# Kernel optimization log

Measured on AMD Instinct MI355X. Metric: run time of the kernel, lower is better.

## Reference

```python
import jax, jax.numpy as jnp
import numpy as np

EPS_COS = 1e-8   # nxn_cos_sim eps
SMOOTH = 1e-4    # DiceLoss smooth
EPS_DICE = 1e-7  # smp soft_dice_score clamp_min eps

BS, C, H, W = 8, 512, 128, 128
K = 512  # codebook / num classes


def setup_inputs() -> dict:
    key = jax.random.key(0)
    k1, k2, k3 = jax.random.split(key, 3)
    output = jax.random.normal(k1, (BS, C, H, W), dtype=jnp.float32)
    embeddings = jax.random.normal(k2, (K, C), dtype=jnp.float32)
    # ground-truth one-hot annotation (bs, K, h, w)
    gt_labels = jax.random.randint(k3, (BS, H, W), 0, K)
    ann_one_hot = jax.nn.one_hot(gt_labels, K, dtype=jnp.float32).transpose(0, 3, 1, 2)
    return {"output": output, "ann_one_hot": ann_one_hot, "embeddings": embeddings}


def reference(output, ann_one_hot, embeddings):
    bs, c, h, w = output.shape
    k = embeddings.shape[0]
    x = output.transpose(0, 2, 3, 1).reshape(-1, c)           # [N, C]
    # nxn cosine similarity [N, K]
    numerator = x @ embeddings.T
    a_l2 = jnp.sum(x * x, axis=1)                              # [N]
    b_l2 = jnp.sum(embeddings * embeddings, axis=1)            # [K]
    denominator = jnp.maximum(jnp.sqrt(a_l2[:, None] * b_l2[None, :]), EPS_COS)
    labels = jnp.argmax(numerator / denominator, axis=-1).reshape(bs, h, w)
    # ann_to_one_hot -> (bs, K, h, w)
    pred_one_hot = jax.nn.one_hot(labels, k, dtype=output.dtype).transpose(0, 3, 1, 2)
    # smp DiceLoss(mode='multilabel', smooth=1e-4, from_logits=False)
    yp = pred_one_hot.reshape(bs, k, -1)
    yt = ann_one_hot.reshape(bs, k, -1).astype(yp.dtype)
    dims = (0, 2)
    intersection = jnp.sum(yp * yt, axis=dims)                 # [K]
    cardinality = jnp.sum(yp + yt, axis=dims)                  # [K]
    score = (2.0 * intersection + SMOOTH) / jnp.maximum(cardinality + SMOOTH, EPS_DICE)
    loss = 1.0 - score
    present = (jnp.sum(yt, axis=dims) > 0).astype(loss.dtype)  # only classes present in GT
    return jnp.mean(loss * present)
```

## Files before the change

### kernel.cpp

```cpp
#include <hip/hip_runtime.h>
#include <hip/hip_bf16.h>

#define BSZ 8
#define CDIM 512
#define KDIM 512
#define HWSZ 16384
#define NPIX (BSZ*HWSZ)

using bf16x8 = __attribute__((ext_vector_type(8))) short;
using f32x4  = __attribute__((ext_vector_type(4))) float;
typedef unsigned long long u64;

__device__ __forceinline__ unsigned pack2bf16(float lo, float hi) {
  return (__builtin_bit_cast(unsigned, lo) >> 16) |
         (__builtin_bit_cast(unsigned, hi) & 0xFFFF0000u);
}

__device__ __forceinline__ void gload_lds16(const unsigned short* g, unsigned short* l) {
  __builtin_amdgcn_global_load_lds(
      (const __attribute__((address_space(1))) unsigned int*)g,
      (__attribute__((address_space(3))) unsigned int*)l, 16, 0, 0);
}

__global__ __launch_bounds__(64) void prep_emb_kernel(const float* __restrict__ E,
                                                      unsigned short* __restrict__ Eb) {
  int k = blockIdx.x;
  int lane = threadIdx.x;
  const float4* row = (const float4*)(E + (size_t)k * CDIM);
  float4 v0 = row[lane * 2], v1 = row[lane * 2 + 1];
  float ss = v0.x*v0.x + v0.y*v0.y + v0.z*v0.z + v0.w*v0.w
           + v1.x*v1.x + v1.y*v1.y + v1.z*v1.z + v1.w*v1.w;
  #pragma unroll
  for (int d = 1; d < 64; d <<= 1) ss += __shfl_xor(ss, d, 64);
  float rinv = rsqrtf(fmaxf(ss, 1e-24f));
  float f[8] = {v0.x, v0.y, v0.z, v0.w, v1.x, v1.y, v1.z, v1.w};
  unsigned o[8];
  #pragma unroll
  for (int e = 0; e < 8; ++e) {
    float x = f[e] * rinv;
    unsigned u = __builtin_bit_cast(unsigned, x);
    o[e] = (u + 0x7FFFu + ((u >> 16) & 1u)) >> 16;
  }
  uint4 pack;
  pack.x = o[0] | (o[1] << 16);
  pack.y = o[2] | (o[3] << 16);
  pack.z = o[4] | (o[5] << 16);
  pack.w = o[6] | (o[7] << 16);
  ((uint4*)(Eb + (size_t)k * CDIM))[lane] = pack;
}

__global__ __launch_bounds__(256) void transpose_gt_kernel(
    const float* __restrict__ X, const float* __restrict__ ANN,
    unsigned short* __restrict__ Xt, float* __restrict__ gt_count) {
  __shared__ unsigned int lds[64 * 65];
  __shared__ float sw[4];
  int t = threadIdx.x;
  int bid = blockIdx.x;
  int pb = bid & 2047, cb = bid >> 11;
  int px0 = pb * 64, c0 = cb * 128;
  int b = px0 >> 14, hw = px0 & (HWSZ - 1);
  int p = t & 15, cg = t >> 4;

  const float* xs = X + ((size_t)b * CDIM + c0) * HWSZ + hw + 4 * p;
  float4 v[8];
  #pragma unroll
  for (int j = 0; j < 4; ++j) {
    const float* s = xs + (size_t)(2 * (cg + 16 * j)) * HWSZ;
    v[2 * j]     = *(const float4*)s;
    v[2 * j + 1] = *(const float4*)(s + HWSZ);
  }
  const float* Ap = ANN + (size_t)bid * 8192 + t * 4;
  float s0 = 0.f;
  #pragma unroll
  for (int r = 0; r < 8; ++r) {
    float4 a4 = *(const float4*)(Ap + r * 1024);
    s0 += (a4.x + a4.y) + (a4.z + a4.w);
  }
  #pragma unroll
  for (int j = 0; j < 4; ++j) {
    float f0[4] = {v[2*j].x, v[2*j].y, v[2*j].z, v[2*j].w};
    float f1[4] = {v[2*j+1].x, v[2*j+1].y, v[2*j+1].z, v[2*j+1].w};
    #pragma unroll
    for (int jj = 0; jj < 4; ++jj)
      lds[(4 * p + jj) * 65 + cg + 16 * j] = pack2bf16(f0[jj], f1[jj]);
  }
  __syncthreads();
  #pragma unroll
  for (int k2 = 0; k2 < 4; ++k2) {
    int ch = t + 256 * k2;
    int px = ch >> 4, j = ch & 15;
    uint4 o;
    o.x = lds[px * 65 + 4 * j];
    o.y = lds[px * 65 + 4 * j + 1];
    o.z = lds[px * 65 + 4 * j + 2];
    o.w = lds[px * 65 + 4 * j + 3];
    *(uint4*)(Xt + (size_t)(px0 + px) * CDIM + c0 + 8 * j) = o;
  }
  #pragma unroll
  for (int d = 1; d < 64; d <<= 1) s0 += __shfl_xor(s0, d, 64);
  if ((t & 63) == 0) sw[t >> 6] = s0;
  __syncthreads();
  if (t == 0) atomicAdd(&gt_count[(bid >> 1) & (KDIM - 1)], sw[0] + sw[1] + sw[2] + sw[3]);
}

__global__ __launch_bounds__(256, 4) void gemm_argmax_kernel(
    const unsigned short* __restrict__ Xt, const unsigned short* __restrict__ Eb,
    u64* __restrict__ keys) {
  __shared__ unsigned short As[2][128 * 32];
  __shared__ unsigned short Bs[2][128 * 32];
  int t = threadIdx.x;
  int lane = t & 63;
  int wv = t >> 6;
  int p15 = lane & 15, q = lane >> 4;
  int wr = wv >> 1, wc = wv & 1;
  int bid = (blockIdx.x & 7) * 512 + (blockIdx.x >> 3);
  int px0  = (bid >> 2) * 128;
  int cls0 = (bid & 3) * 128;

  int ubase = (t & ~63) * 8;
  #define STAGE(buf, i)                                                              \
    {                                                                                \
      _Pragma("unroll")                                                              \
      for (int j = 0; j < 2; ++j) {                                                  \
        int ch = t + 256 * j;                                                        \
        int row = ch >> 2, q4 = ch & 3;                                              \
        gload_lds16(Xt + (size_t)(px0 + row) * CDIM + (i) * 32 + q4 * 8,             \
                    &As[buf][ubase + j * 2048]);                                     \
        gload_lds16(Eb + (size_t)(cls0 + row) * CDIM + (i) * 32 + q4 * 8,            \
                    &Bs[buf][ubase + j * 2048]);                                     \
      }                                                                              \
    }

  f32x4 acc[4][4];
  #pragma unroll
  for (int m = 0; m < 4; ++m)
    #pragma unroll
    for (int n = 0; n < 4; ++n)
      acc[m][n] = (f32x4){0.f, 0.f, 0.f, 0.f};

  STAGE(0, 0);
  for (int i = 0; i < 16; ++i) {
    int cur = i & 1;
    if (i < 15) STAGE(cur ^ 1, i + 1);
    __syncthreads();
    bf16x8 a[4], bfr[4];
    #pragma unroll
    for (int m = 0; m < 4; ++m)
      a[m] = *(bf16x8*)&As[cur][(wr * 64 + m * 16 + p15) * 32 + q * 8];
    #pragma unroll
    for (int n = 0; n < 4; ++n)
      bfr[n] = *(bf16x8*)&Bs[cur][(wc * 64 + n * 16 + p15) * 32 + q * 8];
    #pragma unroll
    for (int n = 0; n < 4; ++n)
      #pragma unroll
      for (int m = 0; m < 4; ++m)
        acc[m][n] = __builtin_amdgcn_mfma_f32_16x16x32_bf16(a[m], bfr[n], acc[m][n], 0, 0, 0);
    __syncthreads();
  }
  #undef STAGE

  #pragma unroll
  for (int m = 0; m < 4; ++m) {
    #pragma unroll
    for (int r = 0; r < 4; ++r) {
      float best = acc[m][0][r];
      int bn = 0;
      #pragma unroll
      for (int n = 1; n < 4; ++n) {
        float v = acc[m][n][r];
        if (v > best) { best = v; bn = n; }
      }
      int bk = cls0 + wc * 64 + bn * 16 + p15;
      #pragma unroll
      for (int d = 1; d < 16; d <<= 1) {
        float ov = __shfl_xor(best, d, 64);
        int   ok = __shfl_xor(bk, d, 64);
        if (ov > best || (ov == best && ok < bk)) { best = ov; bk = ok; }
      }
      if (p15 == 0) {
        int px = px0 + wr * 64 + m * 16 + q * 4 + r;
        unsigned u = __builtin_bit_cast(unsigned, best);
        unsigned ou = u ^ ((unsigned)((int)u >> 31) | 0x80000000u);
        u64 key = ((u64)ou << 32) | (unsigned)(511 - bk);
        atomicMax(&keys[px], key);
      }
    }
  }
}

__global__ __launch_bounds__(256) void count_kernel(
    const u64* __restrict__ keys, const float* __restrict__ ANN,
    int* __restrict__ pred_count, int* __restrict__ inter) {
  int px = blockIdx.x * 256 + threadIdx.x;
  u64 key = keys[px];
  int cls = 511 - (int)(unsigned)(key & 0xFFFFFFFFull);
  atomicAdd(&pred_count[cls], 1);
  int b = px >> 14, hw = px & (HWSZ - 1);
  float g = ANN[((size_t)b * KDIM + cls) * HWSZ + hw];
  if (g > 0.5f) atomicAdd(&inter[cls], 1);
}

__global__ __launch_bounds__(512) void final_kernel(
    const int* __restrict__ pred_count, const int* __restrict__ inter,
    const float* __restrict__ gt_count, float* __restrict__ out) {
  int k = threadIdx.x;
  float G = gt_count[k];
  float P = (float)pred_count[k];
  float I = (float)inter[k];
  float card  = P + G;
  float score = (2.f * I + 1e-4f) / fmaxf(card + 1e-4f, 1e-7f);
  float v = (G > 0.f) ? (1.f - score) : 0.f;
  #pragma unroll
  for (int d = 1; d < 64; d <<= 1) v += __shfl_xor(v, d, 64);
  __shared__ float sw[8];
  if ((k & 63) == 0) sw[k >> 6] = v;
  __syncthreads();
  if (k == 0) {
    float s = 0.f;
    #pragma unroll
    for (int i = 0; i < 8; ++i) s += sw[i];
    out[0] = s / (float)KDIM;
  }
}

__global__ __launch_bounds__(256) void gt_count_fb(const float* __restrict__ ANN,
                                                   float* __restrict__ gt_count) {
  int slice = blockIdx.x;
  int k = slice & (KDIM - 1);
  const float4* p = (const float4*)(ANN + (size_t)slice * HWSZ);
  float s = 0.f;
  #pragma unroll
  for (int i = 0; i < 16; ++i) {
    float4 v = p[threadIdx.x + i * 256];
    s += v.x + v.y + v.z + v.w;
  }
  #pragma unroll
  for (int d = 1; d < 64; d <<= 1) s += __shfl_xor(s, d, 64);
  __shared__ float sw[4];
  if ((threadIdx.x & 63) == 0) sw[threadIdx.x >> 6] = s;
  __syncthreads();
  if (threadIdx.x == 0) atomicAdd(&gt_count[k], sw[0] + sw[1] + sw[2] + sw[3]);
}

__global__ __launch_bounds__(256, 1) void gemm_fb(
    const float* __restrict__ X, const float* __restrict__ ANN,
    const unsigned short* __restrict__ Eb,
    int* __restrict__ pred_count, int* __restrict__ inter) {
  int tid = threadIdx.x;
  int wv = tid >> 6;
  int lane = tid & 63;
  int p15 = lane & 15, q = lane >> 4;
  int pix0 = blockIdx.x * 64;
  int b = pix0 >> 14;
  int hw = pix0 & (HWSZ - 1);
  const float*          Xb = X  + (size_t)b * CDIM * HWSZ + hw + p15;
  const unsigned short* Ew = Eb + (size_t)(wv * 128) * CDIM;
  f32x4 acc[4][8];
  #pragma unroll
  for (int m = 0; m < 4; ++m)
    #pragma unroll
    for (int n = 0; n < 8; ++n)
      acc[m][n] = (f32x4){0.f, 0.f, 0.f, 0.f};
  for (int cs = 0; cs < 16; ++cs) {
    int c0 = cs * 32 + q * 8;
    bf16x8 a[4];
    #pragma unroll
    for (int m = 0; m < 4; ++m)
      #pragma unroll
      for (int e = 0; e < 8; ++e) {
        float x = Xb[(size_t)(c0 + e) * HWSZ + m * 16];
        a[m][e] = (short)(__builtin_bit_cast(unsigned, x) >> 16);
      }
    bf16x8 bfrag[8];
    #pragma unroll
    for (int n = 0; n < 8; ++n)
      bfrag[n] = *(const bf16x8*)(Ew + (size_t)(n * 16 + p15) * CDIM + cs * 32 + q * 8);
    #pragma unroll
    for (int n = 0; n < 8; ++n)
      #pragma unroll
      for (int m = 0; m < 4; ++m)
        acc[m][n] = __builtin_amdgcn_mfma_f32_16x16x32_bf16(a[m], bfrag[n], acc[m][n], 0, 0, 0);
  }
  __shared__ float s_v[4][64];
  __shared__ int   s_k[4][64];
  #pragma unroll
  for (int m = 0; m < 4; ++m)
    #pragma unroll
    for (int r = 0; r < 4; ++r) {
      float best = acc[m][0][r];
      int bn = 0;
      #pragma unroll
      for (int n = 1; n < 8; ++n) {
        float v = acc[m][n][r];
        if (v > best) { best = v; bn = n; }
      }
      int bk = wv * 128 + bn * 16 + p15;
      #pragma unroll
      for (int d = 1; d < 16; d <<= 1) {
        float ov = __shfl_xor(best, d, 64);
        int   ok = __shfl_xor(bk, d, 64);
        if (ov > best || (ov == best && ok < bk)) { best = ov; bk = ok; }
      }
      if (p15 == 0) {
        int p = m * 16 + q * 4 + r;
        s_v[wv][p] = best;
        s_k[wv][p] = bk;
      }
    }
  __syncthreads();
  if (tid < 64) {
    int p = tid;
    float best = s_v[0][p]; int bk = s_k[0][p];
    #pragma unroll
    for (int w = 1; w < 4; ++w) {
      float v = s_v[w][p]; int kk = s_k[w][p];
      if (v > best || (v == best && kk < bk)) { best = v; bk = kk; }
    }
    atomicAdd(&pred_count[bk], 1);
    float g = ANN[((size_t)b * KDIM + bk) * HWSZ + hw + p];
    if (g > 0.5f) atomicAdd(&inter[bk], 1);
  }
}

extern "C" void kernel_launch(void* const* d_in, const int* in_sizes, int n_in,
                              void* d_out, int out_size, void* d_ws, size_t ws_size,
                              hipStream_t stream) {
  const float* X   = (const float*)d_in[0];
  const float* ANN = (const float*)d_in[1];
  const float* E   = (const float*)d_in[2];

  char* base = (char*)d_ws;
  unsigned short* Eb = (unsigned short*)base;
  float* gt_count    = (float*)(base + 524288);
  int*   pred_count  = (int*)  (base + 524288 + 2048);
  int*   inter       = (int*)  (base + 524288 + 4096);
  u64*   keys        = (u64*)  (base + 1048576);
  unsigned short* Xt = (unsigned short*)(base + 2097152);

  size_t need = 2097152 + (size_t)NPIX * CDIM * 2;

  prep_emb_kernel<<<KDIM, 64, 0, stream>>>(E, Eb);
  if (ws_size >= need) {
    hipMemsetAsync(base + 524288, 0, 1048576 + 524288 - 524288 + 1048576, stream);
    transpose_gt_kernel<<<8192, 256, 0, stream>>>(X, ANN, Xt, gt_count);
    gemm_argmax_kernel<<<4096, 256, 0, stream>>>(Xt, Eb, keys);
    count_kernel<<<NPIX / 256, 256, 0, stream>>>(keys, ANN, pred_count, inter);
  } else {
    hipMemsetAsync(base + 524288, 0, 6144, stream);
    gt_count_fb<<<BSZ * KDIM, 256, 0, stream>>>(ANN, gt_count);
    gemm_fb<<<NPIX / 64, 256, 0, stream>>>(X, ANN, Eb, pred_count, inter);
  }
  final_kernel<<<1, 512, 0, stream>>>(pred_count, inter, gt_count, (float*)d_out);
}
```

Baseline: 292.6 us.

## Pre-tile Xt and embeddings into GEMM-block-contiguous layout for linear staging loads

The transpose kernel now writes bf16 activations in a tiled layout, 128-pixel blocks by 32-channel slices stored contiguously. The embedding prep also writes a matching tiled copy. The GEMM staging loads then become fully contiguous 8KB chunks per k-step instead of strided row reads. The transpose kernel is also restructured to 256-pixel by 64-channel tiles, using half as many blocks and a different LDS layout. This costs extra workspace and a second embedding write, and depends on the new index math being correct.

```diff
diff --git a/kernel.cpp b/kernel.cpp
--- a/kernel.cpp
+++ b/kernel.cpp
@@ -23,7 +23,8 @@
 }
 
 __global__ __launch_bounds__(64) void prep_emb_kernel(const float* __restrict__ E,
-                                                      unsigned short* __restrict__ Eb) {
+                                                      unsigned short* __restrict__ Eb,
+                                                      unsigned short* __restrict__ EbT) {
   int k = blockIdx.x;
   int lane = threadIdx.x;
   const float4* row = (const float4*)(E + (size_t)k * CDIM);
@@ -47,64 +48,69 @@
   pack.z = o[4] | (o[5] << 16);
   pack.w = o[6] | (o[7] << 16);
   ((uint4*)(Eb + (size_t)k * CDIM))[lane] = pack;
+  int clsb = k >> 7, rowi = k & 127, cs = lane >> 2, q4 = lane & 3;
+  *(uint4*)(EbT + (size_t)clsb * 65536 + cs * 4096 + rowi * 32 + q4 * 8) = pack;
 }
 
 __global__ __launch_bounds__(256) void transpose_gt_kernel(
     const float* __restrict__ X, const float* __restrict__ ANN,
-    unsigned short* __restrict__ Xt, float* __restrict__ gt_count) {
-  __shared__ unsigned int lds[64 * 65];
-  __shared__ float sw[4];
+    unsigned short* __restrict__ XtT, float* __restrict__ gt_count) {
+  __shared__ unsigned int lds[256 * 36];
+  __shared__ float swr[4];
   int t = threadIdx.x;
   int bid = blockIdx.x;
-  int pb = bid & 2047, cb = bid >> 11;
-  int px0 = pb * 64, c0 = cb * 128;
+  int pt = bid & 511, cg = bid >> 9;
+  int px0 = pt * 256, c0 = cg * 64;
   int b = px0 >> 14, hw = px0 & (HWSZ - 1);
-  int p = t & 15, cg = t >> 4;
-
-  const float* xs = X + ((size_t)b * CDIM + c0) * HWSZ + hw + 4 * p;
-  float4 v[8];
-  #pragma unroll
-  for (int j = 0; j < 4; ++j) {
-    const float* s = xs + (size_t)(2 * (cg + 16 * j)) * HWSZ;
-    v[2 * j]     = *(const float4*)s;
-    v[2 * j + 1] = *(const float4*)(s + HWSZ);
-  }
-  const float* Ap = ANN + (size_t)bid * 8192 + t * 4;
+  int w = t >> 6, lane = t & 63;
+
+  const float* xb = X + ((size_t)b * CDIM + c0 + 16 * w) * HWSZ + hw + 4 * lane;
+  const float* Ap = ANN + (size_t)bid * HWSZ + 4 * t;
   float s0 = 0.f;
-  #pragma unroll
-  for (int r = 0; r < 8; ++r) {
-    float4 a4 = *(const float4*)(Ap + r * 1024);
-    s0 += (a4.x + a4.y) + (a4.z + a4.w);
-  }
-  #pragma unroll
-  for (int j = 0; j < 4; ++j) {
-    float f0[4] = {v[2*j].x, v[2*j].y, v[2*j].z, v[2*j].w};
-    float f1[4] = {v[2*j+1].x, v[2*j+1].y, v[2*j+1].z, v[2*j+1].w};
-    #pragma unroll
-    for (int jj = 0; jj < 4; ++jj)
-      lds[(4 * p + jj) * 65 + cg + 16 * j] = pack2bf16(f0[jj], f1[jj]);
-  }
-  __syncthreads();
-  #pragma unroll
-  for (int k2 = 0; k2 < 4; ++k2) {
-    int ch = t + 256 * k2;
-    int px = ch >> 4, j = ch & 15;
-    uint4 o;
-    o.x = lds[px * 65 + 4 * j];
-    o.y = lds[px * 65 + 4 * j + 1];
-    o.z = lds[px * 65 + 4 * j + 2];
-    o.w = lds[px * 65 + 4 * j + 3];
-    *(uint4*)(Xt + (size_t)(px0 + px) * CDIM + c0 + 8 * j) = o;
+
+  #pragma unroll
+  for (int ph = 0; ph < 2; ++ph) {
+    float4 xv[8];
+    #pragma unroll
+    for (int r = 0; r < 4; ++r) {
+      int cc = 2 * (4 * ph + r);
+      xv[2*r]   = *(const float4*)(xb + (size_t)cc * HWSZ);
+      xv[2*r+1] = *(const float4*)(xb + (size_t)(cc + 1) * HWSZ);
+    }
+    #pragma unroll
+    for (int r = 0; r < 8; ++r) {
+      float4 a4 = *(const float4*)(Ap + (size_t)(8 * ph + r) * 1024);
+      s0 += (a4.x + a4.y) + (a4.z + a4.w);
+    }
+    #pragma unroll
+    for (int j = 0; j < 4; ++j) {
+      unsigned pk[4];
+      #pragma unroll
+      for (int r = 0; r < 4; ++r)
+        pk[r] = pack2bf16(((const float*)&xv[2*r])[j], ((const float*)&xv[2*r+1])[j]);
+      *(uint4*)&lds[(size_t)(4 * lane + j) * 36 + 8 * w + 4 * ph] = *(const uint4*)pk;
+    }
+  }
+  __syncthreads();
+  #pragma unroll
+  for (int rr = 0; rr < 8; ++rr) {
+    int ch = rr * 256 + t;
+    int q4 = ch & 3, px = (ch >> 2) & 255, s = ch >> 10;
+    uint4 o = *(const uint4*)&lds[(size_t)px * 36 + s * 16 + q4 * 4];
+    int pxg = px0 + px;
+    int pxb = pxg >> 7, prow = pxg & 127;
+    int ics = cg * 2 + s;
+    *(uint4*)(XtT + (size_t)(pxb * 16 + ics) * 4096 + prow * 32 + q4 * 8) = o;
   }
   #pragma unroll
   for (int d = 1; d < 64; d <<= 1) s0 += __shfl_xor(s0, d, 64);
-  if ((t & 63) == 0) sw[t >> 6] = s0;
-  __syncthreads();
-  if (t == 0) atomicAdd(&gt_count[(bid >> 1) & (KDIM - 1)], sw[0] + sw[1] + sw[2] + sw[3]);
+  if (lane == 0) swr[w] = s0;
+  __syncthreads();
+  if (t == 0) atomicAdd(&gt_count[bid & (KDIM - 1)], swr[0] + swr[1] + swr[2] + swr[3]);
 }
 
 __global__ __launch_bounds__(256, 4) void gemm_argmax_kernel(
-    const unsigned short* __restrict__ Xt, const unsigned short* __restrict__ Eb,
+    const unsigned short* __restrict__ XtT, const unsigned short* __restrict__ EbT,
     u64* __restrict__ keys) {
   __shared__ unsigned short As[2][128 * 32];
   __shared__ unsigned short Bs[2][128 * 32];
@@ -114,21 +120,22 @@
   int p15 = lane & 15, q = lane >> 4;
   int wr = wv >> 1, wc = wv & 1;
   int bid = (blockIdx.x & 7) * 512 + (blockIdx.x >> 3);
-  int px0  = (bid >> 2) * 128;
-  int cls0 = (bid & 3) * 128;
-
+  int pxb  = bid >> 2;
+  int clsb = bid & 3;
+  int px0  = pxb * 128;
+  int cls0 = clsb * 128;
+
+  const unsigned short* Abase = XtT + (size_t)pxb * 65536;
+  const unsigned short* Bbase = EbT + (size_t)clsb * 65536;
   int ubase = (t & ~63) * 8;
-  #define STAGE(buf, i)                                                              \
-    {                                                                                \
-      _Pragma("unroll")                                                              \
-      for (int j = 0; j < 2; ++j) {                                                  \
-        int ch = t + 256 * j;                                                        \
-        int row = ch >> 2, q4 = ch & 3;                                              \
-        gload_lds16(Xt + (size_t)(px0 + row) * CDIM + (i) * 32 + q4 * 8,             \
-                    &As[buf][ubase + j * 2048]);                                     \
-        gload_lds16(Eb + (size_t)(cls0 + row) * CDIM + (i) * 32 + q4 * 8,            \
-                    &Bs[buf][ubase + j * 2048]);                                     \
-      }                                                                              \
+  #define STAGE(buf, i)                                                       \
+    {                                                                         \
+      _Pragma("unroll")                                                       \
+      for (int j = 0; j < 2; ++j) {                                           \
+        int ch = t + 256 * j;                                                 \
+        gload_lds16(Abase + (size_t)(i) * 4096 + ch * 8, &As[buf][ubase + j * 2048]); \
+        gload_lds16(Bbase + (size_t)(i) * 4096 + ch * 8, &Bs[buf][ubase + j * 2048]); \
+      }                                                                       \
     }
 
   f32x4 acc[4][4];
@@ -330,23 +337,24 @@
   const float* E   = (const float*)d_in[2];
 
   char* base = (char*)d_ws;
-  unsigned short* Eb = (unsigned short*)base;
-  float* gt_count    = (float*)(base + 524288);
-  int*   pred_count  = (int*)  (base + 524288 + 2048);
-  int*   inter       = (int*)  (base + 524288 + 4096);
-  u64*   keys        = (u64*)  (base + 1048576);
-  unsigned short* Xt = (unsigned short*)(base + 2097152);
-
-  size_t need = 2097152 + (size_t)NPIX * CDIM * 2;
-
-  prep_emb_kernel<<<KDIM, 64, 0, stream>>>(E, Eb);
+  unsigned short* Eb  = (unsigned short*)base;
+  unsigned short* EbT = (unsigned short*)(base + 524288);
+  float* gt_count     = (float*)(base + 1048576);
+  int*   pred_count   = (int*)  (base + 1048576 + 2048);
+  int*   inter        = (int*)  (base + 1048576 + 4096);
+  u64*   keys         = (u64*)  (base + 1048576 + 8192);
+  unsigned short* XtT = (unsigned short*)(base + 4194304);
+
+  size_t need = 4194304 + (size_t)NPIX * CDIM * 2;
+
+  prep_emb_kernel<<<KDIM, 64, 0, stream>>>(E, Eb, EbT);
   if (ws_size >= need) {
-    hipMemsetAsync(base + 524288, 0, 1048576 + 524288 - 524288 + 1048576, stream);
-    transpose_gt_kernel<<<8192, 256, 0, stream>>>(X, ANN, Xt, gt_count);
-    gemm_argmax_kernel<<<4096, 256, 0, stream>>>(Xt, Eb, keys);
+    hipMemsetAsync(base + 1048576, 0, 8192 + 1048576, stream);
+    transpose_gt_kernel<<<4096, 256, 0, stream>>>(X, ANN, XtT, gt_count);
+    gemm_argmax_kernel<<<4096, 256, 0, stream>>>(XtT, EbT, keys);
     count_kernel<<<NPIX / 256, 256, 0, stream>>>(keys, ANN, pred_count, inter);
   } else {
-    hipMemsetAsync(base + 524288, 0, 6144, stream);
+    hipMemsetAsync(base + 1048576, 0, 6144, stream);
     gt_count_fb<<<BSZ * KDIM, 256, 0, stream>>>(ANN, gt_count);
     gemm_fb<<<NPIX / 64, 256, 0, stream>>>(X, ANN, Eb, pred_count, inter);
   }
```

After: 277.5 us. -5.1%, faster.
